# Kernel optimization log

Hardware: AMD Instinct MI355X
Metric: run time of the kernel (lower is better)

Reference implementation:

```python
import jax, jax.numpy as jnp
import numpy as np

NUM_HEADS = 4

def setup_inputs() -> dict:
    key = jax.random.key(0)
    ks = jax.random.split(key, 8)
    B, C, H, W = 4, 256, 128, 128
    Cq = C // 8  # query/key channels
    x  = jax.random.normal(ks[0], (B, C, H, W), dtype=jnp.float32)
    Wq = jax.random.normal(ks[1], (Cq, C), dtype=jnp.float32) * 0.05
    bq = jax.random.normal(ks[2], (Cq,),  dtype=jnp.float32) * 0.01
    Wk = jax.random.normal(ks[3], (Cq, C), dtype=jnp.float32) * 0.05
    bk = jax.random.normal(ks[4], (Cq,),  dtype=jnp.float32) * 0.01
    Wv = jax.random.normal(ks[5], (C, C),  dtype=jnp.float32) * 0.05
    bv = jax.random.normal(ks[6], (C,),   dtype=jnp.float32) * 0.01
    # torch init is zeros; use a nonzero value so the attention path contributes
    gamma = jnp.array([0.5], dtype=jnp.float32)
    return {"x": x, "Wq": Wq, "bq": bq, "Wk": Wk, "bk": bk, "Wv": Wv, "bv": bv, "gamma": gamma}

def _conv1x1(x, Wm, b):
    # 1x1 conv == per-pixel linear map over channels
    return jnp.einsum('bchw,oc->bohw', x, Wm) + b[None, :, None, None]

def reference(x, Wq, bq, Wk, bk, Wv, bv, gamma):
    B, C, H, W = x.shape
    nh = NUM_HEADS
    # project, then fold heads into batch: (B*nh, c_head, H, W)
    q = _conv1x1(x, Wq, bq).reshape(B * nh, -1, H, W)
    k = _conv1x1(x, Wk, bk).reshape(B * nh, -1, H, W)
    v = _conv1x1(x, Wv, bv).reshape(B * nh, -1, H, W)
    # horizontal (row-wise) attention over W: energy [BH, H, W, W]
    e_h = jnp.einsum('bchw,bchv->bhwv', q, k)
    a_h = jax.nn.softmax(e_h, axis=-1)
    o_h = jnp.einsum('bhwv,bchv->bchw', a_h, v)  # (BH, cv, H, W)
    # vertical (column-wise) attention over H: energy [BH, W, H, H]
    e_v = jnp.einsum('bchw,bcgw->bwhg', q, k)
    a_v = jax.nn.softmax(e_v, axis=-1)
    # original permutes back as (BH, cv, W, H); requires H == W to add
    o_v = jnp.einsum('bwhg,bcgw->bcwh', a_v, v)
    attn = (o_h + o_v).reshape(B, C, H, W)
    return gamma * attn + x
```

## Files before the change

### kernel.cpp

```cpp
#include <hip/hip_runtime.h>

#define HW 16384

typedef __attribute__((ext_vector_type(8))) short short8;
typedef __attribute__((ext_vector_type(16))) float floatx16;
typedef __attribute__((ext_vector_type(4))) unsigned int uvec4;

__device__ inline unsigned short f2bf(float f) {
    unsigned u = __builtin_bit_cast(unsigned, f);
    u = (u + 0x7FFFu + ((u >> 16) & 1u)) >> 16;
    return (unsigned short)u;
}

__device__ inline unsigned pack_bf_trunc(float lo, float hi) {
    return __builtin_amdgcn_perm(__builtin_bit_cast(unsigned, hi),
                                 __builtin_bit_cast(unsigned, lo), 0x07060302u);
}

__device__ inline unsigned short trunc_bf(float f) {
    return (unsigned short)(__builtin_bit_cast(unsigned, f) >> 16);
}

__global__ __launch_bounds__(256) void cast_xt_kernel(
    const float* __restrict__ x,
    const float* __restrict__ Wq, const float* __restrict__ Wk,
    const float* __restrict__ Wv, unsigned short* __restrict__ Wb,
    unsigned short* __restrict__ xt, unsigned short* __restrict__ xtc)
{
    __shared__ unsigned short T[64][66];
    const int tid = threadIdx.x;
    const int p0 = blockIdx.x * 64;
    const int c0 = blockIdx.y * 64;
    const int b  = blockIdx.z;

    if (b == 0 && blockIdx.y == 0 && blockIdx.x < 80) {
        int e0 = (blockIdx.x * 256 + tid) * 4;
        int row = e0 >> 8, col = e0 & 255;
        const float* src = (row < 32) ? (Wq + row * 256 + col)
                         : (row < 64) ? (Wk + (row - 32) * 256 + col)
                                      : (Wv + (row - 64) * 256 + col);
        float4 v = *(const float4*)src;
        if (row < 32) {
            const float L2E = 1.4426950408889634f;
            v.x *= L2E; v.y *= L2E; v.z *= L2E; v.w *= L2E;
        }
        uint2 pk;
        pk.x = f2bf(v.x) | ((unsigned)f2bf(v.y) << 16);
        pk.y = f2bf(v.z) | ((unsigned)f2bf(v.w) << 16);
        *(uint2*)&Wb[e0] = pk;
    }

    #pragma unroll
    for (int i = 0; i < 4; i++) {
        int e = i * 256 + tid;
        int c = e >> 4, seg = e & 15;
        float4 v = *(const float4*)&x[((b * 256 + c0 + c) << 14) + p0 + seg * 4];
        ((unsigned*)&T[c][seg * 4])[0] = f2bf(v.x) | ((unsigned)f2bf(v.y) << 16);
        ((unsigned*)&T[c][seg * 4])[1] = f2bf(v.z) | ((unsigned)f2bf(v.w) << 16);
    }
    __syncthreads();
    #pragma unroll
    for (int i = 0; i < 2; i++) {
        int e = i * 256 + tid;
        int p = e >> 3, cs = e & 7;
        unsigned short t[8];
        #pragma unroll
        for (int j = 0; j < 8; j++) t[j] = T[cs * 8 + j][p];
        uint4 pk;
        pk.x = t[0] | ((unsigned)t[1] << 16);
        pk.y = t[2] | ((unsigned)t[3] << 16);
        pk.z = t[4] | ((unsigned)t[5] << 16);
        pk.w = t[6] | ((unsigned)t[7] << 16);
        int pix = p0 + p;
        int pT  = ((pix & 127) << 7) | (pix >> 7);
        *(uint4*)&xt [(((b << 14) + pix) << 8) + c0 + cs * 8] = pk;
        *(uint4*)&xtc[(((b << 14) + pT ) << 8) + c0 + cs * 8] = pk;
    }
}

__global__ __launch_bounds__(256, 2) void fused_kernel(
    const unsigned short* __restrict__ Wb, const unsigned short* __restrict__ xt,
    const unsigned short* __restrict__ xtc,
    const float* __restrict__ bq, const float* __restrict__ bk,
    const float* __restrict__ bv,
    const float* __restrict__ xin, const float* __restrict__ gamma,
    float* __restrict__ out)
{
    __shared__ __align__(16) unsigned short XTS[128 * 64];
    __shared__ __align__(16) unsigned short Vs[64 * 128];
    __shared__ __align__(16) unsigned short Kl[128 * 8];
    __shared__ float biasS[80];

    const int tid = threadIdx.x;
    const int logical = (blockIdx.x & 7) * 256 + (blockIdx.x >> 3);
    const int bh = logical & 15, y = logical >> 4;
    const int b = bh >> 2, h = bh & 3;
    const int w = tid >> 6, l = tid & 63, lr = l & 31, lh = l >> 5;
    const int px = 32 * w + lr;

    if (tid < 80) biasS[tid] = (tid < 8)  ? bq[h * 8 + tid] * 1.4426950408889634f
                             : (tid < 16) ? bk[h * 8 + tid - 8]
                                          : bv[h * 64 + tid - 16];

    const int wr0 = (lr < 8)  ? h * 8 + lr
                  : (lr < 16) ? 32 + h * 8 + (lr - 8)
                              : 64 + h * 64 + (lr - 16);
    const int wr1 = 64 + h * 64 + 16 + lr;
    const int wr2 = 64 + h * 64 + 48 + (lr & 15);

    floatx16 z16 = {0,0,0,0,0,0,0,0,0,0,0,0,0,0,0,0};
    short8 z8 = {0,0,0,0,0,0,0,0};
    floatx16 oh0 = z16, oh1 = z16, ov0 = z16, ov1 = z16;
    float ssA = 1.0f, ssB = 1.0f;

    #pragma unroll
    for (int side = 0; side < 2; side++) {
        const unsigned short* xsrc = side ? xtc : xt;
        floatx16 a0 = z16, a1 = z16, a2 = z16;
        for (int kc = 0; kc < 4; kc++) {
            __syncthreads();
            #pragma unroll
            for (int i = 0; i < 4; i++) {
                int e = i * 256 + tid;
                int row = e >> 3, seg = e & 7, cp = seg ^ (row & 7);
                *(uint4*)&XTS[row * 64 + cp * 8] =
                    *(const uint4*)&xsrc[(((b << 14) + y * 128 + row) << 8) + kc * 64 + seg * 8];
            }
            __syncthreads();
            #pragma unroll
            for (int ks = 0; ks < 4; ks++) {
                int cx = ((2 * ks + lh) ^ (lr & 7)) * 8;
                short8 bfr = *(const short8*)&XTS[px * 64 + cx];
                int ck = kc * 64 + (2 * ks + lh) * 8;
                short8 af0 = *(const short8*)&Wb[wr0 * 256 + ck];
                short8 af1 = *(const short8*)&Wb[wr1 * 256 + ck];
                short8 af2 = *(const short8*)&Wb[wr2 * 256 + ck];
                a0 = __builtin_amdgcn_mfma_f32_32x32x16_bf16(af0, bfr, a0, 0, 0, 0);
                a1 = __builtin_amdgcn_mfma_f32_32x32x16_bf16(af1, bfr, a1, 0, 0, 0);
                a2 = __builtin_amdgcn_mfma_f32_32x32x16_bf16(af2, bfr, a2, 0, 0, 0);
            }
        }
        unsigned X0 = pack_bf_trunc(a0[0] + biasS[4 * lh + 0], a0[1] + biasS[4 * lh + 1]);
        unsigned X1 = pack_bf_trunc(a0[2] + biasS[4 * lh + 2], a0[3] + biasS[4 * lh + 3]);
        unsigned pX0 = __shfl_xor(X0, 32), pX1 = __shfl_xor(X1, 32);
        short8 bfq = z8;
        if (lh == 0) {
            uvec4 t; t.x = X0; t.y = X1; t.z = pX0; t.w = pX1;
            bfq = __builtin_bit_cast(short8, t);
        }
        {
            uint2 kk;
            kk.x = pack_bf_trunc(a0[4] + biasS[8 + 4 * lh + 0], a0[5] + biasS[8 + 4 * lh + 1]);
            kk.y = pack_bf_trunc(a0[6] + biasS[8 + 4 * lh + 2], a0[7] + biasS[8 + 4 * lh + 3]);
            *(uint2*)&Kl[px * 8 + 4 * lh] = kk;
        }
        #pragma unroll
        for (int reg = 8; reg < 16; reg++) {
            int ch = (reg & 3) + 8 * ((reg >> 2) - 2) + 4 * lh;
            Vs[ch * 128 + (((px >> 3) ^ (ch & 15)) << 3) + (px & 7)] =
                trunc_bf(a0[reg] + biasS[16 + ch]);
        }
        #pragma unroll
        for (int reg = 0; reg < 16; reg++) {
            int ch = 16 + (reg & 3) + 8 * (reg >> 2) + 4 * lh;
            Vs[ch * 128 + (((px >> 3) ^ (ch & 15)) << 3) + (px & 7)] =
                trunc_bf(a1[reg] + biasS[16 + ch]);
        }
        #pragma unroll
        for (int reg = 0; reg < 8; reg++) {
            int ch = 48 + (reg & 3) + 8 * (reg >> 2) + 4 * lh;
            Vs[ch * 128 + (((px >> 3) ^ (ch & 15)) << 3) + (px & 7)] =
                trunc_bf(a2[reg] + biasS[16 + ch]);
        }
        __syncthreads();
        float partial = 0.f;
        #pragma unroll
        for (int kg = 0; kg < 4; kg++) {
            short8 af = z8;
            if (lh == 0) af = *(const short8*)&Kl[(32 * kg + lr) * 8];
            floatx16 e = __builtin_amdgcn_mfma_f32_32x32x16_bf16(af, bfq, z16, 0, 0, 0);
            #pragma unroll
            for (int r = 0; r < 16; r++) {
                float p = exp2f(e[r]);
                e[r] = p;
                partial += p;
            }
            #pragma unroll
            for (int cc = 0; cc < 2; cc++) {
                unsigned Y0 = pack_bf_trunc(e[8*cc+0], e[8*cc+1]);
                unsigned Y1 = pack_bf_trunc(e[8*cc+2], e[8*cc+3]);
                unsigned Y2 = pack_bf_trunc(e[8*cc+4], e[8*cc+5]);
                unsigned Y3 = pack_bf_trunc(e[8*cc+6], e[8*cc+7]);
                unsigned pY0 = __shfl_xor(Y0, 32);
                unsigned pY1 = __shfl_xor(Y1, 32);
                unsigned pY2 = __shfl_xor(Y2, 32);
                unsigned pY3 = __shfl_xor(Y3, 32);
                uvec4 t;
                t.x = lh ? pY2 : Y0;
                t.y = lh ? pY3 : Y1;
                t.z = lh ? Y2  : pY0;
                t.w = lh ? Y3  : pY1;
                short8 pf = __builtin_bit_cast(short8, t);
                int ks = 2 * kg + cc;
                int cp = ((2 * ks + lh) ^ (lr & 15)) * 8;
                short8 v0 = *(const short8*)&Vs[lr * 128 + cp];
                short8 v1 = *(const short8*)&Vs[(32 + lr) * 128 + cp];
                if (side == 0) {
                    oh0 = __builtin_amdgcn_mfma_f32_32x32x16_bf16(v0, pf, oh0, 0, 0, 0);
                    oh1 = __builtin_amdgcn_mfma_f32_32x32x16_bf16(v1, pf, oh1, 0, 0, 0);
                } else {
                    ov0 = __builtin_amdgcn_mfma_f32_32x32x16_bf16(v0, pf, ov0, 0, 0, 0);
                    ov1 = __builtin_amdgcn_mfma_f32_32x32x16_bf16(v1, pf, ov1, 0, 0, 0);
                }
            }
        }
        float ssum = partial + __shfl_xor(partial, 32);
        if (side == 0) ssA = ssum; else ssB = ssum;
    }

    __syncthreads();

    const float g  = gamma[0];
    const float g0 = g / ssA, g1 = g / ssB;
    #pragma unroll
    for (int reg = 0; reg < 16; reg++) {
        int ch = (reg & 3) + 8 * (reg >> 2) + 4 * lh;
        int idx0 = (bh * 64 + ch) * HW + y * 128 + px;
        int idx1 = (bh * 64 + 32 + ch) * HW + y * 128 + px;
        out[idx0] = g0 * oh0[reg] + g1 * ov0[reg] + xin[idx0];
        out[idx1] = g0 * oh1[reg] + g1 * ov1[reg] + xin[idx1];
    }
}

extern "C" void kernel_launch(void* const* d_in, const int* in_sizes, int n_in,
                              void* d_out, int out_size, void* d_ws, size_t ws_size,
                              hipStream_t stream) {
    const float* x     = (const float*)d_in[0];
    const float* Wq    = (const float*)d_in[1];
    const float* bq    = (const float*)d_in[2];
    const float* Wk    = (const float*)d_in[3];
    const float* bk    = (const float*)d_in[4];
    const float* Wv    = (const float*)d_in[5];
    const float* bv    = (const float*)d_in[6];
    const float* gamma = (const float*)d_in[7];
    float* out = (float*)d_out;

    unsigned short* Wb  = (unsigned short*)d_ws;
    unsigned short* xt  = Wb + 320 * 256;
    unsigned short* xtc = xt + 4 * HW * 256;

    cast_xt_kernel<<<dim3(256, 4, 4), 256, 0, stream>>>(x, Wq, Wk, Wv, Wb, xt, xtc);
    fused_kernel<<<dim3(2048), 256, 0, stream>>>(Wb, xt, xtc, bq, bk, bv, x, gamma, out);
}
```

Measured before the change: 246.4 us.

## Stage per-head weights in LDS and move transposed copy to separate kernel

After: 206.8 us. -16.1%, faster.

```diff
diff --git a/kernel.cpp b/kernel.cpp
--- a/kernel.cpp
+++ b/kernel.cpp
@@ -25,7 +25,7 @@
     const float* __restrict__ x,
     const float* __restrict__ Wq, const float* __restrict__ Wk,
     const float* __restrict__ Wv, unsigned short* __restrict__ Wb,
-    unsigned short* __restrict__ xt, unsigned short* __restrict__ xtc)
+    unsigned short* __restrict__ xt)
 {
     __shared__ unsigned short T[64][66];
     const int tid = threadIdx.x;
@@ -71,10 +71,22 @@
         pk.y = t[2] | ((unsigned)t[3] << 16);
         pk.z = t[4] | ((unsigned)t[5] << 16);
         pk.w = t[6] | ((unsigned)t[7] << 16);
-        int pix = p0 + p;
-        int pT  = ((pix & 127) << 7) | (pix >> 7);
-        *(uint4*)&xt [(((b << 14) + pix) << 8) + c0 + cs * 8] = pk;
-        *(uint4*)&xtc[(((b << 14) + pT ) << 8) + c0 + cs * 8] = pk;
+        *(uint4*)&xt[(((b << 14) + p0 + p) << 8) + c0 + cs * 8] = pk;
+    }
+}
+
+__global__ __launch_bounds__(256) void tpx_kernel(
+    const unsigned short* __restrict__ xt, unsigned short* __restrict__ xtc)
+{
+    const int x0 = blockIdx.x;
+    const int b  = blockIdx.y;
+    const int tid = threadIdx.x;
+    const int r = tid >> 5, cseg = tid & 31;
+    #pragma unroll
+    for (int i = 0; i < 16; i++) {
+        int y = i * 8 + r;
+        uint4 v = *(const uint4*)&xt[(((b << 14) + y * 128 + x0) << 8) + cseg * 8];
+        *(uint4*)&xtc[(((b << 14) + x0 * 128 + y) << 8) + cseg * 8] = v;
     }
 }
 
@@ -86,6 +98,7 @@
     const float* __restrict__ xin, const float* __restrict__ gamma,
     float* __restrict__ out)
 {
+    __shared__ __align__(16) unsigned short Ws[80 * 256];
     __shared__ __align__(16) unsigned short XTS[128 * 64];
     __shared__ __align__(16) unsigned short Vs[64 * 128];
     __shared__ __align__(16) unsigned short Kl[128 * 8];
@@ -102,11 +115,15 @@
                              : (tid < 16) ? bk[h * 8 + tid - 8]
                                           : bv[h * 64 + tid - 16];
 
-    const int wr0 = (lr < 8)  ? h * 8 + lr
-                  : (lr < 16) ? 32 + h * 8 + (lr - 8)
-                              : 64 + h * 64 + (lr - 16);
-    const int wr1 = 64 + h * 64 + 16 + lr;
-    const int wr2 = 64 + h * 64 + 48 + (lr & 15);
+    #pragma unroll
+    for (int i = 0; i < 10; i++) {
+        int e = i * 256 + tid;
+        int R = e >> 5, c = e & 31, cp = c ^ (R & 7);
+        int gr = (R < 8)  ? h * 8 + R
+               : (R < 16) ? 32 + h * 8 + (R - 8)
+                          : 64 + h * 64 + (R - 16);
+        *(uint4*)&Ws[R * 256 + cp * 8] = *(const uint4*)&Wb[gr * 256 + c * 8];
+    }
 
     floatx16 z16 = {0,0,0,0,0,0,0,0,0,0,0,0,0,0,0,0};
     short8 z8 = {0,0,0,0,0,0,0,0};
@@ -131,10 +148,11 @@
             for (int ks = 0; ks < 4; ks++) {
                 int cx = ((2 * ks + lh) ^ (lr & 7)) * 8;
                 short8 bfr = *(const short8*)&XTS[px * 64 + cx];
-                int ck = kc * 64 + (2 * ks + lh) * 8;
-                short8 af0 = *(const short8*)&Wb[wr0 * 256 + ck];
-                short8 af1 = *(const short8*)&Wb[wr1 * 256 + ck];
-                short8 af2 = *(const short8*)&Wb[wr2 * 256 + ck];
+                int ci = kc * 8 + 2 * ks + lh;
+                int cwp = (ci ^ (lr & 7)) * 8;
+                short8 af0 = *(const short8*)&Ws[lr * 256 + cwp];
+                short8 af1 = *(const short8*)&Ws[(32 + lr) * 256 + cwp];
+                short8 af2 = *(const short8*)&Ws[(64 + (lr & 15)) * 256 + cwp];
                 a0 = __builtin_amdgcn_mfma_f32_32x32x16_bf16(af0, bfr, a0, 0, 0, 0);
                 a1 = __builtin_amdgcn_mfma_f32_32x32x16_bf16(af1, bfr, a1, 0, 0, 0);
                 a2 = __builtin_amdgcn_mfma_f32_32x32x16_bf16(af2, bfr, a2, 0, 0, 0);
@@ -249,6 +267,7 @@
     unsigned short* xt  = Wb + 320 * 256;
     unsigned short* xtc = xt + 4 * HW * 256;
 
-    cast_xt_kernel<<<dim3(256, 4, 4), 256, 0, stream>>>(x, Wq, Wk, Wv, Wb, xt, xtc);
+    cast_xt_kernel<<<dim3(256, 4, 4), 256, 0, stream>>>(x, Wq, Wk, Wv, Wb, xt);
+    tpx_kernel<<<dim3(128, 4), 256, 0, stream>>>(xt, xtc);
     fused_kernel<<<dim3(2048), 256, 0, stream>>>(Wb, xt, xtc, bq, bk, bv, x, gamma, out);
 }
```
